# Kernel tuning notes

Measured on AMD Instinct MI355X. Metric: run time of the kernel, lower is better.

## Reference

```python
import jax, jax.numpy as jnp
import numpy as np

N_NODES = 50000
N_EDGES = 800000
IN_DIM = 128
HID_DIM = 128
N_CLASSES = 40


def setup_inputs() -> dict:
    key = jax.random.key(0)
    ks = jax.random.split(key, 12)
    s = 0.05
    inp = {
        "X": jax.random.normal(ks[0], (N_NODES, IN_DIM), jnp.float32),
        "A": jax.random.randint(ks[1], (2, N_EDGES), 0, N_NODES, dtype=jnp.int64),
        "W0": jax.random.normal(ks[2], (HID_DIM, IN_DIM), jnp.float32) * s,
        "b0": jnp.zeros((HID_DIM,), jnp.float32),
        "W1": jax.random.normal(ks[3], (HID_DIM, HID_DIM), jnp.float32) * s,
        "b1": jnp.zeros((HID_DIM,), jnp.float32),
        "W2": jax.random.normal(ks[4], (HID_DIM, HID_DIM), jnp.float32) * s,
        "b2": jnp.zeros((HID_DIM,), jnp.float32),
        "W3": jax.random.normal(ks[5], (HID_DIM, HID_DIM), jnp.float32) * s,
        "b3": jnp.zeros((HID_DIM,), jnp.float32),
        "Wf": jax.random.normal(ks[6], (N_CLASSES, HID_DIM), jnp.float32) * s,
        "bf": jnp.zeros((N_CLASSES,), jnp.float32),
    }
    return inp


def _gcn_conv(x, W, b, src, dst):
    # FrobeniusNormGCNConv: normalize weight by Frobenius norm, then standard GCNConv
    Wn = W / jnp.linalg.norm(W)
    h = x @ Wn.T  # [N, out]
    # gcn_norm with self-loops (edge weight 1.0): deg over targets + 1 self loop
    ones = jnp.ones((dst.shape[0],), h.dtype)
    deg = jax.ops.segment_sum(ones, dst, num_segments=N_NODES) + 1.0
    dinv = jax.lax.rsqrt(deg)  # [N]
    norm = dinv[src] * dinv[dst]  # [E]
    # scatter-add of normalized source messages into targets
    agg = jax.ops.segment_sum(norm[:, None] * h[src], dst, num_segments=N_NODES)
    # self-loop contribution: dinv[i]^2 * h[i]; bias added after aggregation
    return agg + (dinv * dinv)[:, None] * h + b


def reference(X, A, W0, b0, W1, b1, W2, b2, W3, b3, Wf, bf):
    src, dst = A[0], A[1]
    h = _gcn_conv(X, W0, b0, src, dst)
    skip = h
    for W, b in ((W1, b1), (W2, b2), (W3, b3)):
        h = _gcn_conv(h, W, b, src, dst)
        h = jax.nn.relu(h)
        h = h + skip  # residual skip (dropout identity in eval mode)
        skip = h
    return h @ Wf.T + bf
```

## Files before the change

kernel.cpp:

```cpp
#include <hip/hip_runtime.h>

#define N_NODES_C 50000
#define N_EDGES_C 800000
#define DIM 128
#define NCLS 40
#define SCAN_NB ((N_NODES_C + 255) / 256)
#define F2B_NB ((N_NODES_C * DIM / 4) / 256)
#define NBUK 32
#define BCAP 32768

typedef __attribute__((ext_vector_type(8))) short bf16x8;
typedef __attribute__((ext_vector_type(4))) float f32x4;

__device__ inline float bf2f(unsigned short u) {
    union { unsigned int i; float f; } c;
    c.i = ((unsigned int)u) << 16;
    return c.f;
}
__device__ inline unsigned short f2bf(float f) {
    union { float f; unsigned int i; } c;
    c.f = f;
    unsigned int x = c.i;
    x += 0x7fffu + ((x >> 16) & 1u);
    return (unsigned short)(x >> 16);
}
__device__ inline void unp8(const uint4& g, float* f) {
    f[0] = __uint_as_float(g.x << 16); f[1] = __uint_as_float(g.x & 0xFFFF0000u);
    f[2] = __uint_as_float(g.y << 16); f[3] = __uint_as_float(g.y & 0xFFFF0000u);
    f[4] = __uint_as_float(g.z << 16); f[5] = __uint_as_float(g.z & 0xFFFF0000u);
    f[6] = __uint_as_float(g.w << 16); f[7] = __uint_as_float(g.w & 0xFFFF0000u);
}

__global__ __launch_bounds__(256) void k_pre(const float* __restrict__ X,
                                             const float* __restrict__ W0,
                                             const float* __restrict__ W1,
                                             const float* __restrict__ W2,
                                             const float* __restrict__ W3,
                                             unsigned short* __restrict__ Xb,
                                             unsigned short* __restrict__ Wb,
                                             float* __restrict__ scale_inv) {
    int b = blockIdx.x;
    if (b < F2B_NB) {
        int i = b * 256 + threadIdx.x;
        float4 v = reinterpret_cast<const float4*>(X)[i];
        reinterpret_cast<ushort4*>(Xb)[i] =
            make_ushort4(f2bf(v.x), f2bf(v.y), f2bf(v.z), f2bf(v.w));
        return;
    }
    b -= F2B_NB;
    if (b < 64) {
        int m = b >> 4;
        int idx = (b & 15) * 256 + threadIdx.x;
        const float* W = m == 0 ? W0 : m == 1 ? W1 : m == 2 ? W2 : W3;
        float4 v = reinterpret_cast<const float4*>(W)[idx];
        reinterpret_cast<ushort4*>(Wb + (size_t)m * DIM * DIM)[idx] =
            make_ushort4(f2bf(v.x), f2bf(v.y), f2bf(v.z), f2bf(v.w));
        return;
    }
    b -= 64;
    const float* W = b == 0 ? W0 : b == 1 ? W1 : b == 2 ? W2 : W3;
    float s = 0.f;
    for (int i = threadIdx.x; i < DIM * DIM; i += 256) {
        float v = W[i];
        s += v * v;
    }
    #pragma unroll
    for (int off = 32; off >= 1; off >>= 1) s += __shfl_down(s, off);
    __shared__ float red[4];
    int lane = threadIdx.x & 63, wid = threadIdx.x >> 6;
    if (lane == 0) red[wid] = s;
    __syncthreads();
    if (threadIdx.x == 0) {
        float tot = red[0] + red[1] + red[2] + red[3];
        scale_inv[b] = 1.0f / sqrtf(tot);
    }
}

__global__ __launch_bounds__(256) void k_bucket(const int* __restrict__ A,
                                                int* __restrict__ gcount,
                                                unsigned int* __restrict__ ebuk, int E) {
    __shared__ int cnt[NBUK];
    __shared__ int gbase[NBUK];
    int tid = threadIdx.x;
    if (tid < NBUK) cnt[tid] = 0;
    __syncthreads();
    int e0 = blockIdx.x * 1024;
    int s[4], d[4], b[4], r[4];
    #pragma unroll
    for (int j = 0; j < 4; ++j) {
        int e = e0 + j * 256 + tid;
        if (e < E) {
            s[j] = A[e];
            d[j] = A[E + e];
            b[j] = (int)(((unsigned long long)(unsigned)d[j] * NBUK) / N_NODES_C);
            r[j] = atomicAdd(&cnt[b[j]], 1);
        } else {
            b[j] = -1;
        }
    }
    __syncthreads();
    if (tid < NBUK) gbase[tid] = atomicAdd(&gcount[tid], cnt[tid]);
    __syncthreads();
    #pragma unroll
    for (int j = 0; j < 4; ++j) {
        if (b[j] >= 0) {
            int pos = gbase[b[j]] + r[j];
            if (pos < BCAP)
                ebuk[(size_t)b[j] * BCAP + pos] =
                    ((unsigned)d[j] << 16) | (unsigned)s[j];
        }
    }
}

__global__ __launch_bounds__(256) void k_degb(const unsigned int* __restrict__ ebuk,
                                              const int* __restrict__ gcount,
                                              int* __restrict__ deg) {
    int k = blockIdx.x;
    int base = (k * N_NODES_C + NBUK - 1) / NBUK;
    int next = ((k + 1) * N_NODES_C + NBUK - 1) / NBUK;
    int sz = next - base;
    __shared__ int dl[1568];
    for (int i = threadIdx.x; i < sz; i += 256) dl[i] = 0;
    __syncthreads();
    int count = gcount[k];
    if (count > BCAP) count = BCAP;
    for (int i = threadIdx.x; i < count; i += 256) {
        int d = (int)(ebuk[(size_t)k * BCAP + i] >> 16);
        atomicAdd(&dl[d - base], 1);
    }
    __syncthreads();
    for (int i = threadIdx.x; i < sz; i += 256) deg[base + i] = dl[i];
}

__global__ __launch_bounds__(256) void k_scan_part(const int* __restrict__ cnt,
                                                   int* __restrict__ partial,
                                                   float* __restrict__ dinv,
                                                   int* __restrict__ fill, int n) {
    int idx = blockIdx.x * 256 + threadIdx.x;
    int v = (idx < n) ? cnt[idx] : 0;
    if (idx < n) {
        dinv[idx] = rsqrtf((float)v + 1.0f);
        fill[idx] = 0;
    }
    int s = v;
    #pragma unroll
    for (int off = 32; off >= 1; off >>= 1) s += __shfl_down(s, off);
    __shared__ int red[4];
    int lane = threadIdx.x & 63, wid = threadIdx.x >> 6;
    if (lane == 0) red[wid] = s;
    __syncthreads();
    if (threadIdx.x == 0) partial[blockIdx.x] = red[0] + red[1] + red[2] + red[3];
}

__global__ __launch_bounds__(256) void k_scan_final(const int* __restrict__ cnt,
                                                    const int* __restrict__ partial,
                                                    int* __restrict__ ptr, int n, int nb) {
    int tid = threadIdx.x, bid = blockIdx.x;
    int lane = tid & 63, wid = tid >> 6;
    int pv = (tid < nb) ? partial[tid] : 0;
    int vb = (tid < bid) ? pv : 0;
    int s1 = vb, s2 = pv;
    #pragma unroll
    for (int off = 32; off >= 1; off >>= 1) {
        s1 += __shfl_down(s1, off);
        s2 += __shfl_down(s2, off);
    }
    __shared__ int r1[4], r2[4];
    if (lane == 0) { r1[wid] = s1; r2[wid] = s2; }
    __syncthreads();
    __shared__ int sbase, stot;
    if (tid == 0) {
        sbase = r1[0] + r1[1] + r1[2] + r1[3];
        stot  = r2[0] + r2[1] + r2[2] + r2[3];
    }
    __syncthreads();
    int idx = bid * 256 + tid;
    int v = (idx < n) ? cnt[idx] : 0;
    int sc = v;
    #pragma unroll
    for (int off = 1; off < 64; off <<= 1) {
        int t = __shfl_up(sc, off);
        if (lane >= off) sc += t;
    }
    __shared__ int wsum[4], wpre[4];
    if (lane == 63) wsum[wid] = sc;
    __syncthreads();
    if (tid == 0) {
        int acc = 0;
        #pragma unroll
        for (int w = 0; w < 4; ++w) { wpre[w] = acc; acc += wsum[w]; }
    }
    __syncthreads();
    if (idx < n) ptr[idx] = sbase + wpre[wid] + sc - v;
    if (bid == 0 && tid == 0) ptr[n] = stot;
}

__global__ __launch_bounds__(256) void k_fillb(const unsigned int* __restrict__ ebuk,
                                               const int* __restrict__ gcount,
                                               const int* __restrict__ ptr,
                                               int* __restrict__ fill,
                                               unsigned short* __restrict__ esrc) {
    int k = blockIdx.x & (NBUK - 1);
    int c = blockIdx.x / NBUK;
    int count = gcount[k];
    if (count > BCAP) count = BCAP;
    int i0 = c * 1024;
    if (i0 >= count) return;
    #pragma unroll
    for (int j = 0; j < 4; ++j) {
        int i = i0 + j * 256 + threadIdx.x;
        if (i < count) {
            unsigned v = ebuk[(size_t)k * BCAP + i];
            int d = (int)(v >> 16);
            int s = (int)(v & 0xFFFFu);
            int pos = ptr[d] + atomicAdd(&fill[d], 1);
            esrc[pos] = (unsigned short)s;
        }
    }
}

__global__ __launch_bounds__(256) void k_gemm_mfma(const unsigned short* __restrict__ Xb,
                                                   const unsigned short* __restrict__ Wb,
                                                   const float* __restrict__ scale_ptr,
                                                   const float* __restrict__ dinv,
                                                   unsigned short* __restrict__ Gb, int N) {
    int tid = threadIdx.x;
    int w = tid >> 6;
    int l = tid & 63;
    int l15 = l & 15;
    int lg = l >> 4;
    int arow = blockIdx.x * 64 + w * 16 + l15;
    if (arow >= N) arow = N - 1;
    float scale = scale_ptr[0];

    f32x4 acc[8];
    #pragma unroll
    for (int ct = 0; ct < 8; ++ct) acc[ct] = f32x4{0.f, 0.f, 0.f, 0.f};

    #pragma unroll
    for (int kc = 0; kc < 4; ++kc) {
        int ko = kc * 32 + lg * 8;
        bf16x8 a = *reinterpret_cast<const bf16x8*>(&Xb[(size_t)arow * DIM + ko]);
        #pragma unroll
        for (int ct = 0; ct < 8; ++ct) {
            bf16x8 b = *reinterpret_cast<const bf16x8*>(&Wb[(size_t)(ct * 16 + l15) * DIM + ko]);
            acc[ct] = __builtin_amdgcn_mfma_f32_16x16x32_bf16(a, b, acc[ct], 0, 0, 0);
        }
    }
    int outrow0 = blockIdx.x * 64 + w * 16 + lg * 4;
    #pragma unroll
    for (int r = 0; r < 4; ++r) {
        int row = outrow0 + r;
        if (row < N) {
            float dv = dinv[row] * scale;
            #pragma unroll
            for (int ct = 0; ct < 8; ++ct)
                Gb[(size_t)row * DIM + ct * 16 + l15] = f2bf(acc[ct][r] * dv);
        }
    }
}

__global__ __launch_bounds__(256) void k_agg(const unsigned short* __restrict__ Gb,
                                             const float* __restrict__ bias,
                                             const float* __restrict__ dinv,
                                             const int* __restrict__ ptr,
                                             const unsigned short* __restrict__ esrc,
                                             const unsigned short* __restrict__ skipb,
                                             unsigned short* __restrict__ outb,
                                             int relu_res, int N) {
    int n = blockIdx.x * 4 + (threadIdx.x >> 6);
    if (n >= N) return;
    int l = threadIdx.x & 63;
    int grp = l >> 4, li = l & 15;
    const uint4* __restrict__ Gv = reinterpret_cast<const uint4*>(Gb);
    int beg = ptr[n], end = ptr[n + 1];
    float acc[8] = {};
    float t[8];
    int e = beg;
    for (; e + 8 <= end; e += 8) {
        int s0 = esrc[e + grp];
        int s1 = esrc[e + 4 + grp];
        uint4 g0 = Gv[(size_t)s0 * 16 + li];
        uint4 g1 = Gv[(size_t)s1 * 16 + li];
        unp8(g0, t);
        #pragma unroll
        for (int j = 0; j < 8; ++j) acc[j] += t[j];
        unp8(g1, t);
        #pragma unroll
        for (int j = 0; j < 8; ++j) acc[j] += t[j];
    }
    for (; e + 4 <= end; e += 4) {
        int s0 = esrc[e + grp];
        uint4 g0 = Gv[(size_t)s0 * 16 + li];
        unp8(g0, t);
        #pragma unroll
        for (int j = 0; j < 8; ++j) acc[j] += t[j];
    }
    int rem = end - e;
    if (grp < rem) {
        int s0 = esrc[e + grp];
        uint4 g0 = Gv[(size_t)s0 * 16 + li];
        unp8(g0, t);
        #pragma unroll
        for (int j = 0; j < 8; ++j) acc[j] += t[j];
    }
    #pragma unroll
    for (int j = 0; j < 8; ++j) {
        acc[j] += __shfl_xor(acc[j], 16);
        acc[j] += __shfl_xor(acc[j], 32);
    }
    if (grp == 0) {
        float di = dinv[n];
        uint4 gu = Gv[(size_t)n * 16 + li];
        float gs[8];
        unp8(gu, gs);
        const float4* b4 = reinterpret_cast<const float4*>(bias);
        float4 ba = b4[li * 2], bb = b4[li * 2 + 1];
        float bv[8] = {ba.x, ba.y, ba.z, ba.w, bb.x, bb.y, bb.z, bb.w};
        float v[8];
        #pragma unroll
        for (int j = 0; j < 8; ++j) v[j] = fmaf(di, acc[j] + gs[j], bv[j]);
        if (relu_res) {
            uint4 su = reinterpret_cast<const uint4*>(skipb)[(size_t)n * 16 + li];
            float ss[8];
            unp8(su, ss);
            #pragma unroll
            for (int j = 0; j < 8; ++j) v[j] = fmaxf(v[j], 0.f) + ss[j];
        }
        uint4 o;
        o.x = (unsigned)f2bf(v[0]) | ((unsigned)f2bf(v[1]) << 16);
        o.y = (unsigned)f2bf(v[2]) | ((unsigned)f2bf(v[3]) << 16);
        o.z = (unsigned)f2bf(v[4]) | ((unsigned)f2bf(v[5]) << 16);
        o.w = (unsigned)f2bf(v[6]) | ((unsigned)f2bf(v[7]) << 16);
        reinterpret_cast<uint4*>(outb)[(size_t)n * 16 + li] = o;
    }
}

__global__ __launch_bounds__(256) void k_final(const unsigned short* __restrict__ Hb,
                                               const float* __restrict__ Wf,
                                               const float* __restrict__ bf,
                                               float* __restrict__ out, int N) {
    __shared__ float Xs[16][68];
    __shared__ float Ws[16][64];
    int tid = threadIdx.x;
    int n0 = blockIdx.x * 64;
    int tx = tid & 15;
    int ty = tid >> 4;
    float acc[4][4] = {};
    for (int k0 = 0; k0 < DIM; k0 += 16) {
        {
            int j = tid >> 2, kq = tid & 3;
            int row = n0 + j;
            if (row >= N) row = N - 1;
            ushort4 x4 = *reinterpret_cast<const ushort4*>(&Hb[(size_t)row * DIM + k0 + kq * 4]);
            Xs[kq * 4 + 0][j] = bf2f(x4.x);
            Xs[kq * 4 + 1][j] = bf2f(x4.y);
            Xs[kq * 4 + 2][j] = bf2f(x4.z);
            Xs[kq * 4 + 3][j] = bf2f(x4.w);
        }
        {
            int o = tid >> 2, kq = tid & 3;
            int om = o < NCLS ? o : o - NCLS;
            const float4 w4 = *reinterpret_cast<const float4*>(&Wf[(size_t)om * DIM + k0 + kq * 4]);
            Ws[kq * 4 + 0][o] = w4.x;
            Ws[kq * 4 + 1][o] = w4.y;
            Ws[kq * 4 + 2][o] = w4.z;
            Ws[kq * 4 + 3][o] = w4.w;
        }
        __syncthreads();
        #pragma unroll
        for (int k = 0; k < 16; ++k) {
            float4 w = *reinterpret_cast<const float4*>(&Ws[k][tx * 4]);
            float4 x = *reinterpret_cast<const float4*>(&Xs[k][ty * 4]);
            float xv[4] = {x.x, x.y, x.z, x.w};
            #pragma unroll
            for (int i = 0; i < 4; ++i) {
                acc[i][0] = fmaf(xv[i], w.x, acc[i][0]);
                acc[i][1] = fmaf(xv[i], w.y, acc[i][1]);
                acc[i][2] = fmaf(xv[i], w.z, acc[i][2]);
                acc[i][3] = fmaf(xv[i], w.w, acc[i][3]);
            }
        }
        __syncthreads();
    }
    if (tx >= 10) return;
    float4 b4 = make_float4(bf[tx * 4], bf[tx * 4 + 1], bf[tx * 4 + 2], bf[tx * 4 + 3]);
    #pragma unroll
    for (int i = 0; i < 4; ++i) {
        int row = n0 + ty * 4 + i;
        if (row < N) {
            float* op = &out[(size_t)row * NCLS + tx * 4];
            op[0] = acc[i][0] + b4.x;
            op[1] = acc[i][1] + b4.y;
            op[2] = acc[i][2] + b4.z;
            op[3] = acc[i][3] + b4.w;
        }
    }
}

extern "C" void kernel_launch(void* const* d_in, const int* in_sizes, int n_in,
                              void* d_out, int out_size, void* d_ws, size_t ws_size,
                              hipStream_t stream) {
    (void)in_sizes; (void)n_in; (void)out_size; (void)ws_size;
    const float* X  = (const float*)d_in[0];
    const int*   A  = (const int*)d_in[1];
    const float* W0 = (const float*)d_in[2];
    const float* b0 = (const float*)d_in[3];
    const float* W1 = (const float*)d_in[4];
    const float* b1 = (const float*)d_in[5];
    const float* W2 = (const float*)d_in[6];
    const float* b2 = (const float*)d_in[7];
    const float* W3 = (const float*)d_in[8];
    const float* b3 = (const float*)d_in[9];
    const float* Wf = (const float*)d_in[10];
    const float* bf = (const float*)d_in[11];
    float* out = (float*)d_out;

    char* base_ws = (char*)d_ws;
    size_t off = 0;
    auto alloc = [&](size_t bytes) -> char* {
        char* p = base_ws + off;
        off = (off + bytes + 255) & ~(size_t)255;
        return p;
    };
    float* scale_inv = (float*)alloc(4 * sizeof(float));
    int*   deg    = (int*)alloc(N_NODES_C * sizeof(int));
    int*   fill   = (int*)alloc(N_NODES_C * sizeof(int));
    int*   ptr    = (int*)alloc((N_NODES_C + 1) * sizeof(int));
    float* dinv   = (float*)alloc(N_NODES_C * sizeof(float));
    int*   part   = (int*)alloc(SCAN_NB * sizeof(int));
    int*   gcount = (int*)alloc(NBUK * sizeof(int));
    unsigned int*   ebuk = (unsigned int*)alloc((size_t)NBUK * BCAP * sizeof(unsigned int));
    unsigned short* esrc = (unsigned short*)alloc((size_t)N_EDGES_C * sizeof(unsigned short));
    unsigned short* Gb  = (unsigned short*)alloc((size_t)N_NODES_C * DIM * sizeof(unsigned short));
    unsigned short* Xb  = (unsigned short*)alloc((size_t)N_NODES_C * DIM * sizeof(unsigned short));
    unsigned short* Hb1 = (unsigned short*)alloc((size_t)N_NODES_C * DIM * sizeof(unsigned short));
    unsigned short* Hb2 = (unsigned short*)alloc((size_t)N_NODES_C * DIM * sizeof(unsigned short));
    unsigned short* Wb  = (unsigned short*)alloc((size_t)4 * DIM * DIM * sizeof(unsigned short));

    hipMemsetAsync(gcount, 0, NBUK * sizeof(int), stream);

    k_pre<<<F2B_NB + 64 + 4, 256, 0, stream>>>(X, W0, W1, W2, W3, Xb, Wb, scale_inv);
    k_bucket<<<(N_EDGES_C + 1023) / 1024, 256, 0, stream>>>(A, gcount, ebuk, N_EDGES_C);
    k_degb<<<NBUK, 256, 0, stream>>>(ebuk, gcount, deg);
    k_scan_part<<<SCAN_NB, 256, 0, stream>>>(deg, part, dinv, fill, N_NODES_C);
    k_scan_final<<<SCAN_NB, 256, 0, stream>>>(deg, part, ptr, N_NODES_C, SCAN_NB);
    k_fillb<<<NBUK * (BCAP / 1024), 256, 0, stream>>>(ebuk, gcount, ptr, fill, esrc);

    const int gemm_grid = (N_NODES_C + 63) / 64;
    const int agg_grid  = (N_NODES_C + 3) / 4;

    k_gemm_mfma<<<gemm_grid, 256, 0, stream>>>(Xb, Wb + 0 * DIM * DIM, scale_inv + 0, dinv, Gb, N_NODES_C);
    k_agg<<<agg_grid, 256, 0, stream>>>(Gb, b0, dinv, ptr, esrc, nullptr, Hb1, 0, N_NODES_C);
    k_gemm_mfma<<<gemm_grid, 256, 0, stream>>>(Hb1, Wb + 1 * DIM * DIM, scale_inv + 1, dinv, Gb, N_NODES_C);
    k_agg<<<agg_grid, 256, 0, stream>>>(Gb, b1, dinv, ptr, esrc, Hb1, Hb2, 1, N_NODES_C);
    k_gemm_mfma<<<gemm_grid, 256, 0, stream>>>(Hb2, Wb + 2 * DIM * DIM, scale_inv + 2, dinv, Gb, N_NODES_C);
    k_agg<<<agg_grid, 256, 0, stream>>>(Gb, b2, dinv, ptr, esrc, Hb2, Hb1, 1, N_NODES_C);
    k_gemm_mfma<<<gemm_grid, 256, 0, stream>>>(Hb1, Wb + 3 * DIM * DIM, scale_inv + 3, dinv, Gb, N_NODES_C);
    k_agg<<<agg_grid, 256, 0, stream>>>(Gb, b3, dinv, ptr, esrc, Hb1, Hb2, 1, N_NODES_C);
    k_final<<<(N_NODES_C + 63) / 64, 256, 0, stream>>>(Hb2, Wf, bf, out, N_NODES_C);
}
```

Measured before the change: 353.9 us.

## Fuse X conversion into GEMM, final linear into last aggregation, drop memset

The first GEMM now reads the fp32 input directly and converts it to bf16 in registers, which removes the separate conversion pass and the Xb buffer. The final 128->40 linear layer is folded into the last aggregation kernel by staging each node's fp32 row in shared memory, so the last hidden layer is never written out in bf16. The gcount memset moves into k_pre, and the aggregation gather loop is unrolled to 16 edges. The fused final layer reloads Wf for every 4-node block and adds a __syncthreads, and the unchecked bounds rely on N_NODES being divisible by 4.

```diff
diff --git a/kernel.cpp b/kernel.cpp
--- a/kernel.cpp
+++ b/kernel.cpp
@@ -5,7 +5,6 @@
 #define DIM 128
 #define NCLS 40
 #define SCAN_NB ((N_NODES_C + 255) / 256)
-#define F2B_NB ((N_NODES_C * DIM / 4) / 256)
 #define NBUK 32
 #define BCAP 32768
 
@@ -31,23 +30,14 @@
     f[6] = __uint_as_float(g.w << 16); f[7] = __uint_as_float(g.w & 0xFFFF0000u);
 }
 
-__global__ __launch_bounds__(256) void k_pre(const float* __restrict__ X,
-                                             const float* __restrict__ W0,
+__global__ __launch_bounds__(256) void k_pre(const float* __restrict__ W0,
                                              const float* __restrict__ W1,
                                              const float* __restrict__ W2,
                                              const float* __restrict__ W3,
-                                             unsigned short* __restrict__ Xb,
                                              unsigned short* __restrict__ Wb,
-                                             float* __restrict__ scale_inv) {
+                                             float* __restrict__ scale_inv,
+                                             int* __restrict__ gcount) {
     int b = blockIdx.x;
-    if (b < F2B_NB) {
-        int i = b * 256 + threadIdx.x;
-        float4 v = reinterpret_cast<const float4*>(X)[i];
-        reinterpret_cast<ushort4*>(Xb)[i] =
-            make_ushort4(f2bf(v.x), f2bf(v.y), f2bf(v.z), f2bf(v.w));
-        return;
-    }
-    b -= F2B_NB;
     if (b < 64) {
         int m = b >> 4;
         int idx = (b & 15) * 256 + threadIdx.x;
@@ -58,6 +48,7 @@
         return;
     }
     b -= 64;
+    if (b == 0 && threadIdx.x < NBUK) gcount[threadIdx.x] = 0;
     const float* W = b == 0 ? W0 : b == 1 ? W1 : b == 2 ? W2 : W3;
     float s = 0.f;
     for (int i = threadIdx.x; i < DIM * DIM; i += 256) {
@@ -219,7 +210,8 @@
     }
 }
 
-__global__ __launch_bounds__(256) void k_gemm_mfma(const unsigned short* __restrict__ Xb,
+template <bool F32A>
+__global__ __launch_bounds__(256) void k_gemm_mfma(const void* __restrict__ Xp,
                                                    const unsigned short* __restrict__ Wb,
                                                    const float* __restrict__ scale_ptr,
                                                    const float* __restrict__ dinv,
@@ -240,7 +232,19 @@
     #pragma unroll
     for (int kc = 0; kc < 4; ++kc) {
         int ko = kc * 32 + lg * 8;
-        bf16x8 a = *reinterpret_cast<const bf16x8*>(&Xb[(size_t)arow * DIM + ko]);
+        bf16x8 a;
+        if (F32A) {
+            const float4* xf = reinterpret_cast<const float4*>(
+                (const float*)Xp + (size_t)arow * DIM + ko);
+            float4 u = xf[0], v = xf[1];
+            a[0] = (short)f2bf(u.x); a[1] = (short)f2bf(u.y);
+            a[2] = (short)f2bf(u.z); a[3] = (short)f2bf(u.w);
+            a[4] = (short)f2bf(v.x); a[5] = (short)f2bf(v.y);
+            a[6] = (short)f2bf(v.z); a[7] = (short)f2bf(v.w);
+        } else {
+            a = *reinterpret_cast<const bf16x8*>(
+                (const unsigned short*)Xp + (size_t)arow * DIM + ko);
+        }
         #pragma unroll
         for (int ct = 0; ct < 8; ++ct) {
             bf16x8 b = *reinterpret_cast<const bf16x8*>(&Wb[(size_t)(ct * 16 + l15) * DIM + ko]);
@@ -260,6 +264,7 @@
     }
 }
 
+template <int MODE>
 __global__ __launch_bounds__(256) void k_agg(const unsigned short* __restrict__ Gb,
                                              const float* __restrict__ bias,
                                              const float* __restrict__ dinv,
@@ -267,9 +272,12 @@
                                              const unsigned short* __restrict__ esrc,
                                              const unsigned short* __restrict__ skipb,
                                              unsigned short* __restrict__ outb,
-                                             int relu_res, int N) {
-    int n = blockIdx.x * 4 + (threadIdx.x >> 6);
-    if (n >= N) return;
+                                             const float* __restrict__ Wf,
+                                             const float* __restrict__ bf,
+                                             float* __restrict__ outf) {
+    __shared__ float hstage[4][DIM];
+    int nloc = threadIdx.x >> 6;
+    int n = blockIdx.x * 4 + nloc;
     int l = threadIdx.x & 63;
     int grp = l >> 4, li = l & 15;
     const uint4* __restrict__ Gv = reinterpret_cast<const uint4*>(Gb);
@@ -277,15 +285,25 @@
     float acc[8] = {};
     float t[8];
     int e = beg;
-    for (; e + 8 <= end; e += 8) {
+    for (; e + 16 <= end; e += 16) {
         int s0 = esrc[e + grp];
         int s1 = esrc[e + 4 + grp];
+        int s2 = esrc[e + 8 + grp];
+        int s3 = esrc[e + 12 + grp];
         uint4 g0 = Gv[(size_t)s0 * 16 + li];
         uint4 g1 = Gv[(size_t)s1 * 16 + li];
+        uint4 g2 = Gv[(size_t)s2 * 16 + li];
+        uint4 g3 = Gv[(size_t)s3 * 16 + li];
         unp8(g0, t);
         #pragma unroll
         for (int j = 0; j < 8; ++j) acc[j] += t[j];
         unp8(g1, t);
+        #pragma unroll
+        for (int j = 0; j < 8; ++j) acc[j] += t[j];
+        unp8(g2, t);
+        #pragma unroll
+        for (int j = 0; j < 8; ++j) acc[j] += t[j];
+        unp8(g3, t);
         #pragma unroll
         for (int j = 0; j < 8; ++j) acc[j] += t[j];
     }
@@ -320,80 +338,41 @@
         float v[8];
         #pragma unroll
         for (int j = 0; j < 8; ++j) v[j] = fmaf(di, acc[j] + gs[j], bv[j]);
-        if (relu_res) {
+        if (MODE >= 1) {
             uint4 su = reinterpret_cast<const uint4*>(skipb)[(size_t)n * 16 + li];
             float ss[8];
             unp8(su, ss);
             #pragma unroll
             for (int j = 0; j < 8; ++j) v[j] = fmaxf(v[j], 0.f) + ss[j];
         }
-        uint4 o;
-        o.x = (unsigned)f2bf(v[0]) | ((unsigned)f2bf(v[1]) << 16);
-        o.y = (unsigned)f2bf(v[2]) | ((unsigned)f2bf(v[3]) << 16);
-        o.z = (unsigned)f2bf(v[4]) | ((unsigned)f2bf(v[5]) << 16);
-        o.w = (unsigned)f2bf(v[6]) | ((unsigned)f2bf(v[7]) << 16);
-        reinterpret_cast<uint4*>(outb)[(size_t)n * 16 + li] = o;
-    }
-}
-
-__global__ __launch_bounds__(256) void k_final(const unsigned short* __restrict__ Hb,
-                                               const float* __restrict__ Wf,
-                                               const float* __restrict__ bf,
-                                               float* __restrict__ out, int N) {
-    __shared__ float Xs[16][68];
-    __shared__ float Ws[16][64];
-    int tid = threadIdx.x;
-    int n0 = blockIdx.x * 64;
-    int tx = tid & 15;
-    int ty = tid >> 4;
-    float acc[4][4] = {};
-    for (int k0 = 0; k0 < DIM; k0 += 16) {
-        {
-            int j = tid >> 2, kq = tid & 3;
-            int row = n0 + j;
-            if (row >= N) row = N - 1;
-            ushort4 x4 = *reinterpret_cast<const ushort4*>(&Hb[(size_t)row * DIM + k0 + kq * 4]);
-            Xs[kq * 4 + 0][j] = bf2f(x4.x);
-            Xs[kq * 4 + 1][j] = bf2f(x4.y);
-            Xs[kq * 4 + 2][j] = bf2f(x4.z);
-            Xs[kq * 4 + 3][j] = bf2f(x4.w);
-        }
-        {
-            int o = tid >> 2, kq = tid & 3;
-            int om = o < NCLS ? o : o - NCLS;
-            const float4 w4 = *reinterpret_cast<const float4*>(&Wf[(size_t)om * DIM + k0 + kq * 4]);
-            Ws[kq * 4 + 0][o] = w4.x;
-            Ws[kq * 4 + 1][o] = w4.y;
-            Ws[kq * 4 + 2][o] = w4.z;
-            Ws[kq * 4 + 3][o] = w4.w;
-        }
+        if (MODE == 2) {
+            #pragma unroll
+            for (int j = 0; j < 8; ++j) hstage[nloc][li * 8 + j] = v[j];
+        } else {
+            uint4 o;
+            o.x = (unsigned)f2bf(v[0]) | ((unsigned)f2bf(v[1]) << 16);
+            o.y = (unsigned)f2bf(v[2]) | ((unsigned)f2bf(v[3]) << 16);
+            o.z = (unsigned)f2bf(v[4]) | ((unsigned)f2bf(v[5]) << 16);
+            o.w = (unsigned)f2bf(v[6]) | ((unsigned)f2bf(v[7]) << 16);
+            reinterpret_cast<uint4*>(outb)[(size_t)n * 16 + li] = o;
+        }
+    }
+    if (MODE == 2) {
         __syncthreads();
-        #pragma unroll
-        for (int k = 0; k < 16; ++k) {
-            float4 w = *reinterpret_cast<const float4*>(&Ws[k][tx * 4]);
-            float4 x = *reinterpret_cast<const float4*>(&Xs[k][ty * 4]);
-            float xv[4] = {x.x, x.y, x.z, x.w};
+        int tidx = threadIdx.x;
+        if (tidx < 4 * NCLS) {
+            int nl = tidx / NCLS;
+            int o = tidx - nl * NCLS;
+            const float4* wp = reinterpret_cast<const float4*>(&Wf[(size_t)o * DIM]);
+            const float4* hp = reinterpret_cast<const float4*>(&hstage[nl][0]);
+            float s = 0.f;
             #pragma unroll
-            for (int i = 0; i < 4; ++i) {
-                acc[i][0] = fmaf(xv[i], w.x, acc[i][0]);
-                acc[i][1] = fmaf(xv[i], w.y, acc[i][1]);
-                acc[i][2] = fmaf(xv[i], w.z, acc[i][2]);
-                acc[i][3] = fmaf(xv[i], w.w, acc[i][3]);
+            for (int k = 0; k < DIM / 4; ++k) {
+                float4 wv = wp[k];
+                float4 hv = hp[k];
+                s += wv.x * hv.x + wv.y * hv.y + wv.z * hv.z + wv.w * hv.w;
             }
-        }
-        __syncthreads();
-    }
-    if (tx >= 10) return;
-    float4 b4 = make_float4(bf[tx * 4], bf[tx * 4 + 1], bf[tx * 4 + 2], bf[tx * 4 + 3]);
-    #pragma unroll
-    for (int i = 0; i < 4; ++i) {
-        int row = n0 + ty * 4 + i;
-        if (row < N) {
-            float* op = &out[(size_t)row * NCLS + tx * 4];
-            op[0] = acc[i][0] + b4.x;
-            op[1] = acc[i][1] + b4.y;
-            op[2] = acc[i][2] + b4.z;
-            op[3] = acc[i][3] + b4.w;
+            outf[(size_t)(blockIdx.x * 4 + nl) * NCLS + o] = s + bf[o];
         }
     }
 }
@@ -433,14 +412,11 @@
     unsigned int*   ebuk = (unsigned int*)alloc((size_t)NBUK * BCAP * sizeof(unsigned int));
     unsigned short* esrc = (unsigned short*)alloc((size_t)N_EDGES_C * sizeof(unsigned short));
     unsigned short* Gb  = (unsigned short*)alloc((size_t)N_NODES_C * DIM * sizeof(unsigned short));
-    unsigned short* Xb  = (unsigned short*)alloc((size_t)N_NODES_C * DIM * sizeof(unsigned short));
     unsigned short* Hb1 = (unsigned short*)alloc((size_t)N_NODES_C * DIM * sizeof(unsigned short));
     unsigned short* Hb2 = (unsigned short*)alloc((size_t)N_NODES_C * DIM * sizeof(unsigned short));
     unsigned short* Wb  = (unsigned short*)alloc((size_t)4 * DIM * DIM * sizeof(unsigned short));
 
-    hipMemsetAsync(gcount, 0, NBUK * sizeof(int), stream);
-
-    k_pre<<<F2B_NB + 64 + 4, 256, 0, stream>>>(X, W0, W1, W2, W3, Xb, Wb, scale_inv);
+    k_pre<<<68, 256, 0, stream>>>(W0, W1, W2, W3, Wb, scale_inv, gcount);
     k_bucket<<<(N_EDGES_C + 1023) / 1024, 256, 0, stream>>>(A, gcount, ebuk, N_EDGES_C);
     k_degb<<<NBUK, 256, 0, stream>>>(ebuk, gcount, deg);
     k_scan_part<<<SCAN_NB, 256, 0, stream>>>(deg, part, dinv, fill, N_NODES_C);
@@ -448,15 +424,14 @@
     k_fillb<<<NBUK * (BCAP / 1024), 256, 0, stream>>>(ebuk, gcount, ptr, fill, esrc);
 
     const int gemm_grid = (N_NODES_C + 63) / 64;
-    const int agg_grid  = (N_NODES_C + 3) / 4;
-
-    k_gemm_mfma<<<gemm_grid, 256, 0, stream>>>(Xb, Wb + 0 * DIM * DIM, scale_inv + 0, dinv, Gb, N_NODES_C);
-    k_agg<<<agg_grid, 256, 0, stream>>>(Gb, b0, dinv, ptr, esrc, nullptr, Hb1, 0, N_NODES_C);
-    k_gemm_mfma<<<gemm_grid, 256, 0, stream>>>(Hb1, Wb + 1 * DIM * DIM, scale_inv + 1, dinv, Gb, N_NODES_C);
-    k_agg<<<agg_grid, 256, 0, stream>>>(Gb, b1, dinv, ptr, esrc, Hb1, Hb2, 1, N_NODES_C);
-    k_gemm_mfma<<<gemm_grid, 256, 0, stream>>>(Hb2, Wb + 2 * DIM * DIM, scale_inv + 2, dinv, Gb, N_NODES_C);
-    k_agg<<<agg_grid, 256, 0, stream>>>(Gb, b2, dinv, ptr, esrc, Hb2, Hb1, 1, N_NODES_C);
-    k_gemm_mfma<<<gemm_grid, 256, 0, stream>>>(Hb1, Wb + 3 * DIM * DIM, scale_inv + 3, dinv, Gb, N_NODES_C);
-    k_agg<<<agg_grid, 256, 0, stream>>>(Gb, b3, dinv, ptr, esrc, Hb1, Hb2, 1, N_NODES_C);
-    k_final<<<(N_NODES_C + 63) / 64, 256, 0, stream>>>(Hb2, Wf, bf, out, N_NODES_C);
-}
+    const int agg_grid  = N_NODES_C / 4;
+
+    k_gemm_mfma<true><<<gemm_grid, 256, 0, stream>>>(X, Wb + 0 * DIM * DIM, scale_inv + 0, dinv, Gb, N_NODES_C);
+    k_agg<0><<<agg_grid, 256, 0, stream>>>(Gb, b0, dinv, ptr, esrc, nullptr, Hb1, nullptr, nullptr, nullptr);
+    k_gemm_mfma<false><<<gemm_grid, 256, 0, stream>>>(Hb1, Wb + 1 * DIM * DIM, scale_inv + 1, dinv, Gb, N_NODES_C);
+    k_agg<1><<<agg_grid, 256, 0, stream>>>(Gb, b1, dinv, ptr, esrc, Hb1, Hb2, nullptr, nullptr, nullptr);
+    k_gemm_mfma<false><<<gemm_grid, 256, 0, stream>>>(Hb2, Wb + 2 * DIM * DIM, scale_inv + 2, dinv, Gb, N_NODES_C);
+    k_agg<1><<<agg_grid, 256, 0, stream>>>(Gb, b2, dinv, ptr, esrc, Hb2, Hb1, nullptr, nullptr, nullptr);
+    k_gemm_mfma<false><<<gemm_grid, 256, 0, stream>>>(Hb1, Wb + 3 * DIM * DIM, scale_inv + 3, dinv, Gb, N_NODES_C);
+    k_agg<2><<<agg_grid, 256, 0, stream>>>(Gb, b3, dinv, ptr, esrc, Hb1, nullptr, Wf, bf, out);
+}
```

Measured after the change: 427.4 us. 20.8% more time.

## Fuse X fp32-to-bf16 conversion into first GEMM, unroll aggregation, drop memset

Applied to the files above, without the earlier changes.

Removes the separate pass that converted X to bf16. The first GEMM now reads fp32 X directly and converts it in registers, which saves a 25.6MB read and a 12.8MB write/read round trip. The gcount memset moves into k_pre, which removes one API call. The aggregation gather loop is unrolled to 16 edges per iteration for more memory-level parallelism, and the relu flag and bounds check are templated or removed. The changes add register pressure in k_agg, and the first GEMM now issues wider fp32 loads.

```diff
diff --git a/kernel.cpp b/kernel.cpp
--- a/kernel.cpp
+++ b/kernel.cpp
@@ -5,7 +5,6 @@
 #define DIM 128
 #define NCLS 40
 #define SCAN_NB ((N_NODES_C + 255) / 256)
-#define F2B_NB ((N_NODES_C * DIM / 4) / 256)
 #define NBUK 32
 #define BCAP 32768
 
@@ -31,23 +30,14 @@
     f[6] = __uint_as_float(g.w << 16); f[7] = __uint_as_float(g.w & 0xFFFF0000u);
 }
 
-__global__ __launch_bounds__(256) void k_pre(const float* __restrict__ X,
-                                             const float* __restrict__ W0,
+__global__ __launch_bounds__(256) void k_pre(const float* __restrict__ W0,
                                              const float* __restrict__ W1,
                                              const float* __restrict__ W2,
                                              const float* __restrict__ W3,
-                                             unsigned short* __restrict__ Xb,
                                              unsigned short* __restrict__ Wb,
-                                             float* __restrict__ scale_inv) {
+                                             float* __restrict__ scale_inv,
+                                             int* __restrict__ gcount) {
     int b = blockIdx.x;
-    if (b < F2B_NB) {
-        int i = b * 256 + threadIdx.x;
-        float4 v = reinterpret_cast<const float4*>(X)[i];
-        reinterpret_cast<ushort4*>(Xb)[i] =
-            make_ushort4(f2bf(v.x), f2bf(v.y), f2bf(v.z), f2bf(v.w));
-        return;
-    }
-    b -= F2B_NB;
     if (b < 64) {
         int m = b >> 4;
         int idx = (b & 15) * 256 + threadIdx.x;
@@ -58,6 +48,7 @@
         return;
     }
     b -= 64;
+    if (b == 0 && threadIdx.x < NBUK) gcount[threadIdx.x] = 0;
     const float* W = b == 0 ? W0 : b == 1 ? W1 : b == 2 ? W2 : W3;
     float s = 0.f;
     for (int i = threadIdx.x; i < DIM * DIM; i += 256) {
@@ -219,7 +210,8 @@
     }
 }
 
-__global__ __launch_bounds__(256) void k_gemm_mfma(const unsigned short* __restrict__ Xb,
+template <bool F32A>
+__global__ __launch_bounds__(256) void k_gemm_mfma(const void* __restrict__ Xp,
                                                    const unsigned short* __restrict__ Wb,
                                                    const float* __restrict__ scale_ptr,
                                                    const float* __restrict__ dinv,
@@ -240,7 +232,19 @@
     #pragma unroll
     for (int kc = 0; kc < 4; ++kc) {
         int ko = kc * 32 + lg * 8;
-        bf16x8 a = *reinterpret_cast<const bf16x8*>(&Xb[(size_t)arow * DIM + ko]);
+        bf16x8 a;
+        if (F32A) {
+            const float4* xf = reinterpret_cast<const float4*>(
+                (const float*)Xp + (size_t)arow * DIM + ko);
+            float4 u = xf[0], v = xf[1];
+            a[0] = (short)f2bf(u.x); a[1] = (short)f2bf(u.y);
+            a[2] = (short)f2bf(u.z); a[3] = (short)f2bf(u.w);
+            a[4] = (short)f2bf(v.x); a[5] = (short)f2bf(v.y);
+            a[6] = (short)f2bf(v.z); a[7] = (short)f2bf(v.w);
+        } else {
+            a = *reinterpret_cast<const bf16x8*>(
+                (const unsigned short*)Xp + (size_t)arow * DIM + ko);
+        }
         #pragma unroll
         for (int ct = 0; ct < 8; ++ct) {
             bf16x8 b = *reinterpret_cast<const bf16x8*>(&Wb[(size_t)(ct * 16 + l15) * DIM + ko]);
@@ -260,16 +264,15 @@
     }
 }
 
+template <bool RELU>
 __global__ __launch_bounds__(256) void k_agg(const unsigned short* __restrict__ Gb,
                                              const float* __restrict__ bias,
                                              const float* __restrict__ dinv,
                                              const int* __restrict__ ptr,
                                              const unsigned short* __restrict__ esrc,
                                              const unsigned short* __restrict__ skipb,
-                                             unsigned short* __restrict__ outb,
-                                             int relu_res, int N) {
+                                             unsigned short* __restrict__ outb) {
     int n = blockIdx.x * 4 + (threadIdx.x >> 6);
-    if (n >= N) return;
     int l = threadIdx.x & 63;
     int grp = l >> 4, li = l & 15;
     const uint4* __restrict__ Gv = reinterpret_cast<const uint4*>(Gb);
@@ -277,15 +280,25 @@
     float acc[8] = {};
     float t[8];
     int e = beg;
-    for (; e + 8 <= end; e += 8) {
+    for (; e + 16 <= end; e += 16) {
         int s0 = esrc[e + grp];
         int s1 = esrc[e + 4 + grp];
+        int s2 = esrc[e + 8 + grp];
+        int s3 = esrc[e + 12 + grp];
         uint4 g0 = Gv[(size_t)s0 * 16 + li];
         uint4 g1 = Gv[(size_t)s1 * 16 + li];
+        uint4 g2 = Gv[(size_t)s2 * 16 + li];
+        uint4 g3 = Gv[(size_t)s3 * 16 + li];
         unp8(g0, t);
         #pragma unroll
         for (int j = 0; j < 8; ++j) acc[j] += t[j];
         unp8(g1, t);
+        #pragma unroll
+        for (int j = 0; j < 8; ++j) acc[j] += t[j];
+        unp8(g2, t);
+        #pragma unroll
+        for (int j = 0; j < 8; ++j) acc[j] += t[j];
+        unp8(g3, t);
         #pragma unroll
         for (int j = 0; j < 8; ++j) acc[j] += t[j];
     }
@@ -320,7 +333,7 @@
         float v[8];
         #pragma unroll
         for (int j = 0; j < 8; ++j) v[j] = fmaf(di, acc[j] + gs[j], bv[j]);
-        if (relu_res) {
+        if (RELU) {
             uint4 su = reinterpret_cast<const uint4*>(skipb)[(size_t)n * 16 + li];
             float ss[8];
             unp8(su, ss);
@@ -433,14 +446,11 @@
     unsigned int*   ebuk = (unsigned int*)alloc((size_t)NBUK * BCAP * sizeof(unsigned int));
     unsigned short* esrc = (unsigned short*)alloc((size_t)N_EDGES_C * sizeof(unsigned short));
     unsigned short* Gb  = (unsigned short*)alloc((size_t)N_NODES_C * DIM * sizeof(unsigned short));
-    unsigned short* Xb  = (unsigned short*)alloc((size_t)N_NODES_C * DIM * sizeof(unsigned short));
     unsigned short* Hb1 = (unsigned short*)alloc((size_t)N_NODES_C * DIM * sizeof(unsigned short));
     unsigned short* Hb2 = (unsigned short*)alloc((size_t)N_NODES_C * DIM * sizeof(unsigned short));
     unsigned short* Wb  = (unsigned short*)alloc((size_t)4 * DIM * DIM * sizeof(unsigned short));
 
-    hipMemsetAsync(gcount, 0, NBUK * sizeof(int), stream);
-
-    k_pre<<<F2B_NB + 64 + 4, 256, 0, stream>>>(X, W0, W1, W2, W3, Xb, Wb, scale_inv);
+    k_pre<<<68, 256, 0, stream>>>(W0, W1, W2, W3, Wb, scale_inv, gcount);
     k_bucket<<<(N_EDGES_C + 1023) / 1024, 256, 0, stream>>>(A, gcount, ebuk, N_EDGES_C);
     k_degb<<<NBUK, 256, 0, stream>>>(ebuk, gcount, deg);
     k_scan_part<<<SCAN_NB, 256, 0, stream>>>(deg, part, dinv, fill, N_NODES_C);
@@ -448,15 +458,15 @@
     k_fillb<<<NBUK * (BCAP / 1024), 256, 0, stream>>>(ebuk, gcount, ptr, fill, esrc);
 
     const int gemm_grid = (N_NODES_C + 63) / 64;
-    const int agg_grid  = (N_NODES_C + 3) / 4;
-
-    k_gemm_mfma<<<gemm_grid, 256, 0, stream>>>(Xb, Wb + 0 * DIM * DIM, scale_inv + 0, dinv, Gb, N_NODES_C);
-    k_agg<<<agg_grid, 256, 0, stream>>>(Gb, b0, dinv, ptr, esrc, nullptr, Hb1, 0, N_NODES_C);
-    k_gemm_mfma<<<gemm_grid, 256, 0, stream>>>(Hb1, Wb + 1 * DIM * DIM, scale_inv + 1, dinv, Gb, N_NODES_C);
-    k_agg<<<agg_grid, 256, 0, stream>>>(Gb, b1, dinv, ptr, esrc, Hb1, Hb2, 1, N_NODES_C);
-    k_gemm_mfma<<<gemm_grid, 256, 0, stream>>>(Hb2, Wb + 2 * DIM * DIM, scale_inv + 2, dinv, Gb, N_NODES_C);
-    k_agg<<<agg_grid, 256, 0, stream>>>(Gb, b2, dinv, ptr, esrc, Hb2, Hb1, 1, N_NODES_C);
-    k_gemm_mfma<<<gemm_grid, 256, 0, stream>>>(Hb1, Wb + 3 * DIM * DIM, scale_inv + 3, dinv, Gb, N_NODES_C);
-    k_agg<<<agg_grid, 256, 0, stream>>>(Gb, b3, dinv, ptr, esrc, Hb1, Hb2, 1, N_NODES_C);
+    const int agg_grid  = N_NODES_C / 4;
+
+    k_gemm_mfma<true><<<gemm_grid, 256, 0, stream>>>(X, Wb + 0 * DIM * DIM, scale_inv + 0, dinv, Gb, N_NODES_C);
+    k_agg<false><<<agg_grid, 256, 0, stream>>>(Gb, b0, dinv, ptr, esrc, nullptr, Hb1);
+    k_gemm_mfma<false><<<gemm_grid, 256, 0, stream>>>(Hb1, Wb + 1 * DIM * DIM, scale_inv + 1, dinv, Gb, N_NODES_C);
+    k_agg<true><<<agg_grid, 256, 0, stream>>>(Gb, b1, dinv, ptr, esrc, Hb1, Hb2);
+    k_gemm_mfma<false><<<gemm_grid, 256, 0, stream>>>(Hb2, Wb + 2 * DIM * DIM, scale_inv + 2, dinv, Gb, N_NODES_C);
+    k_agg<true><<<agg_grid, 256, 0, stream>>>(Gb, b2, dinv, ptr, esrc, Hb2, Hb1);
+    k_gemm_mfma<false><<<gemm_grid, 256, 0, stream>>>(Hb1, Wb + 3 * DIM * DIM, scale_inv + 3, dinv, Gb, N_NODES_C);
+    k_agg<true><<<agg_grid, 256, 0, stream>>>(Gb, b3, dinv, ptr, esrc, Hb1, Hb2);
     k_final<<<(N_NODES_C + 63) / 64, 256, 0, stream>>>(Hb2, Wf, bf, out, N_NODES_C);
 }
```

After: 340.1 us. 1.04x faster.
